# Kernel tuning notes

Measured on AMD Instinct MI355X. Metric: run time of the kernel, lower is better.

Reference implementation:

```python
import jax, jax.numpy as jnp
import numpy as np

B, T, D, V, MEM = 2, 512, 512, 256, 256


def _gru(x, h0, wih, whh, bih, bhh):
    # x: [B,T,D], h0: [B,D]; torch GRU gate order: r, z, n
    def step(h, xt):
        gi = xt @ wih.T + bih            # [B,3D]
        gh = h @ whh.T + bhh             # [B,3D]
        i_r, i_z, i_n = jnp.split(gi, 3, axis=-1)
        h_r, h_z, h_n = jnp.split(gh, 3, axis=-1)
        r = jax.nn.sigmoid(i_r + h_r)
        z = jax.nn.sigmoid(i_z + h_z)
        n = jnp.tanh(i_n + r * h_n)
        h_new = (1.0 - z) * n + z * h
        return h_new, h_new
    hT, ys = jax.lax.scan(step, h0, jnp.swapaxes(x, 0, 1))
    return jnp.swapaxes(ys, 0, 1), hT


def _layernorm(x, g, b, eps=1e-5):
    m = jnp.mean(x, axis=-1, keepdims=True)
    v = jnp.mean((x - m) ** 2, axis=-1, keepdims=True)
    return (x - m) / jnp.sqrt(v + eps) * g + b


def setup_inputs() -> dict:
    key = jax.random.key(0)
    ks = jax.random.split(key, 24)
    s = 1.0 / np.sqrt(D)
    inp = {
        'x': jax.random.randint(ks[0], (B, T), 0, V, dtype=jnp.int32),
        'h_f': jnp.zeros((1, B, D), jnp.float32),
        'h_s': jnp.zeros((1, B, D), jnp.float32),
        'soma_w': jax.random.normal(ks[1], (V, D), jnp.float32),
        'fast_wih': jax.random.normal(ks[2], (3 * D, D)) * s,
        'fast_whh': jax.random.normal(ks[3], (3 * D, D)) * s,
        'fast_bih': jax.random.normal(ks[4], (3 * D,)) * s,
        'fast_bhh': jax.random.normal(ks[5], (3 * D,)) * s,
        'slow_wih': jax.random.normal(ks[6], (3 * D, D)) * s,
        'slow_whh': jax.random.normal(ks[7], (3 * D, D)) * s,
        'slow_bih': jax.random.normal(ks[8], (3 * D,)) * s,
        'slow_bhh': jax.random.normal(ks[9], (3 * D,)) * s,
        'qkv_w': jax.random.normal(ks[10], (3 * D, D)) * s,
        'qkv_b': jax.random.normal(ks[11], (3 * D,)) * s,
        'gate_w': jax.random.normal(ks[12], (D, D)) * s,
        'gate_b': jax.random.normal(ks[13], (D,)) * s,
        'gate_g': jnp.ones((D,), jnp.float32),
        'gate_bb': jnp.zeros((D,), jnp.float32),
        'mem_bank': jax.random.normal(ks[14], (MEM, D)) * 0.1,
        'hip_qw': jax.random.normal(ks[15], (D, D)) * s,
        'hip_qb': jax.random.normal(ks[16], (D,)) * s,
        'axon_w': jax.random.normal(ks[17], (D, 4 * D)) * (0.5 * s),
        'axon_b': jax.random.normal(ks[18], (D,)) * s,
        'norm_g': jnp.ones((D,), jnp.float32),
        'norm_b': jnp.zeros((D,), jnp.float32),
    }
    return inp


def reference(x, h_f, h_s, soma_w, fast_wih, fast_whh, fast_bih, fast_bhh,
              slow_wih, slow_whh, slow_bih, slow_bhh, qkv_w, qkv_b,
              gate_w, gate_b, gate_g, gate_bb, mem_bank, hip_qw, hip_qb,
              axon_w, axon_b, norm_g, norm_b):
    d = soma_w.shape[1]
    s_in = soma_w[x]  # mod[0] == 1.0
    p_f, hf1 = _gru(s_in, h_f[0], fast_wih, fast_whh, fast_bih, fast_bhh)
    p_s, hs1 = _gru(p_f, h_s[0], slow_wih, slow_whh, slow_bih, slow_bhh)
    # LinearIntentMemory: naive cumulative outer-product linear attention
    qkv = p_s @ qkv_w.T + qkv_b
    q, k, v = jnp.split(qkv, 3, axis=-1)
    q = jax.nn.elu(q) + 1.0
    k = jax.nn.elu(k) + 1.0
    kv_cum = jnp.cumsum(jnp.einsum('bti,btj->btij', k, v), axis=1)  # [B,T,D,D]
    num = jnp.einsum('bti,btij->btj', q, kv_cum)
    den = jnp.einsum('bti,bti->bt', q, jnp.cumsum(k, axis=1))[..., None] + 1e-6
    l_mem = num / den
    # intent gate: Linear -> LayerNorm -> Tanh
    intent = jnp.tanh(_layernorm(p_s @ gate_w.T + gate_b, gate_g, gate_bb))
    # hippocampus: softmax attention over memory bank
    qh = p_s @ hip_qw.T + hip_qb
    attn = qh @ mem_bank.T / jnp.sqrt(jnp.float32(d))
    episodes = jax.nn.softmax(attn, axis=-1) @ mem_bank
    combined = jnp.concatenate([p_f, intent, l_mem, episodes], axis=-1)
    thought = _layernorm(jnp.tanh(combined @ axon_w.T + axon_b), norm_g, norm_b)
    sw = soma_w / jnp.maximum(jnp.linalg.norm(soma_w, axis=-1, keepdims=True), 1e-12)
    logits = (thought @ sw.T) * 16.0
    return (logits, thought, hf1[None], hs1[None])
```

## Files before the change

kernel.cpp:

```cpp
#include <hip/hip_runtime.h>
#include <cstddef>

#define F_ELUQK 1
#define F_CAUSAL 2
#define F_DIV 4
#define F_NN 8
#define F_SCALE 16
#define F_ROWSUM 32
#define FLAG_STRIDE 32
#define L_WGS 64
#define UNITS 8

enum : int {
  OFF_QH = 0,
  OFF_COMB = 524288,
  OFF_PS = OFF_COMB + 2097152,
  OFF_QKV = OFF_PS + 524288,
  OFF_SCORES = OFF_QKV + 1572864,
  OFF_DEN = OFF_SCORES + 524288,
  OFF_TMP = OFF_DEN + 1024,
  OFF_ATTN = OFF_TMP + 524288,
  OFF_SWN = OFF_ATTN + 262144,
  OFF_RING = OFF_SWN + 256,
  OFF_HSB = OFF_RING + 4096,
  OFF_FLAGS = OFF_HSB + 2048
};

__global__ __launch_bounds__(256) void gemm(
    const float* __restrict__ A, int lda, const float* __restrict__ B, int ldb,
    float* __restrict__ C, int ldc, int coff, int K,
    const float* __restrict__ bias, const float* __restrict__ den,
    const float* __restrict__ cscale, float* __restrict__ rsum,
    float scale, int flags, int bBatch,
    float* __restrict__ Cz, int kzoff) {
  __shared__ float As[16 * 65];
  __shared__ float Bs[16 * 65];
  int tid = threadIdx.x;
  int n0 = blockIdx.x * 64, m0 = blockIdx.y * 64;
  if (blockIdx.z) { A += kzoff; B += kzoff; C = Cz; bias = nullptr; }
  int rowoff = (m0 >> 9) * bBatch;
  int tx = tid & 15, ty = tid >> 4;

  if ((flags & F_CAUSAL) && n0 > ((m0 & 511) + 63)) {
    #pragma unroll
    for (int i = 0; i < 4; ++i)
      #pragma unroll
      for (int j = 0; j < 4; ++j)
        C[(size_t)(m0 + ty * 4 + i) * ldc + coff + n0 + tx * 4 + j] = 0.f;
    return;
  }

  float acc[4][4] = {};
  for (int k0 = 0; k0 < K; k0 += 16) {
    {
      int rr = tid >> 2, c4 = (tid & 3) << 2;
      const float* ap = A + (size_t)(m0 + rr) * lda + (k0 + c4);
      float4 av = *(const float4*)ap;
      As[(c4 + 0) * 65 + rr] = av.x;
      As[(c4 + 1) * 65 + rr] = av.y;
      As[(c4 + 2) * 65 + rr] = av.z;
      As[(c4 + 3) * 65 + rr] = av.w;
    }
    if (!(flags & F_NN)) {
      int rr = tid >> 2, c4 = (tid & 3) << 2;
      const float* bp = B + (size_t)(n0 + rr + rowoff) * ldb + (k0 + c4);
      float4 bv = *(const float4*)bp;
      Bs[(c4 + 0) * 65 + rr] = bv.x; Bs[(c4 + 1) * 65 + rr] = bv.y;
      Bs[(c4 + 2) * 65 + rr] = bv.z; Bs[(c4 + 3) * 65 + rr] = bv.w;
    } else {
      int kk = tid >> 4, n4 = (tid & 15) << 2;
      const float* bp = B + (size_t)(k0 + kk + rowoff) * ldb + (n0 + n4);
      float4 bv = *(const float4*)bp;
      Bs[kk * 65 + n4 + 0] = bv.x; Bs[kk * 65 + n4 + 1] = bv.y;
      Bs[kk * 65 + n4 + 2] = bv.z; Bs[kk * 65 + n4 + 3] = bv.w;
    }
    __syncthreads();
    #pragma unroll
    for (int k = 0; k < 16; ++k) {
      float av[4], bv[4];
      #pragma unroll
      for (int i = 0; i < 4; ++i) av[i] = As[k * 65 + ty * 4 + i];
      #pragma unroll
      for (int j = 0; j < 4; ++j) bv[j] = Bs[k * 65 + tx * 4 + j];
      #pragma unroll
      for (int i = 0; i < 4; ++i)
        #pragma unroll
        for (int j = 0; j < 4; ++j)
          acc[i][j] = fmaf(av[i], bv[j], acc[i][j]);
    }
    __syncthreads();
  }
  float rs[4] = {0.f, 0.f, 0.f, 0.f};
  #pragma unroll
  for (int i = 0; i < 4; ++i) {
    int m = m0 + ty * 4 + i;
    float dv = (flags & F_DIV) ? (1.0f / (den[m] + 1e-6f)) : 1.0f;
    #pragma unroll
    for (int j = 0; j < 4; ++j) {
      int n = n0 + tx * 4 + j;
      float v = acc[i][j];
      if (bias) v += bias[n];
      if (flags & F_ELUQK) { if (n < 1024) v = (v > 0.f) ? (v + 1.f) : __expf(v); }
      if (flags & F_CAUSAL) { if (n > (m & 511)) v = 0.f; }
      if (flags & F_SCALE) v *= scale;
      if (cscale) v *= cscale[coff + n];
      if (flags & F_DIV) v *= dv;
      C[(size_t)m * ldc + coff + n] = v;
      if (flags & F_ROWSUM) rs[i] += v;
    }
  }
  if (flags & F_ROWSUM) {
    #pragma unroll
    for (int i = 0; i < 4; ++i) {
      float s = rs[i];
      s += __shfl_xor(s, 1); s += __shfl_xor(s, 2);
      s += __shfl_xor(s, 4); s += __shfl_xor(s, 8);
      if (tx == 0) atomicAdd(rsum + (m0 + ty * 4 + i), s);
    }
  }
}

__global__ __launch_bounds__(256) void gemm3(
    const float* __restrict__ A,
    const float* __restrict__ qkvw, const float* __restrict__ qkvb,
    const float* __restrict__ gatew, const float* __restrict__ gateb,
    const float* __restrict__ hipw, const float* __restrict__ hipb,
    float* __restrict__ QKV, float* __restrict__ TMP, float* __restrict__ QH) {
  __shared__ float As[16 * 65];
  __shared__ float Bs[16 * 65];
  int tid = threadIdx.x;
  int n0 = blockIdx.x * 64, m0 = blockIdx.y * 64;
  const float* B; const float* bias; float* C; int ldc, base;
  if (n0 < 1536) { B = qkvw; bias = qkvb; C = QKV; ldc = 1536; base = 0; }
  else if (n0 < 2048) { B = gatew; bias = gateb; C = TMP; ldc = 512; base = 1536; }
  else { B = hipw; bias = hipb; C = QH; ldc = 512; base = 2048; }
  int tx = tid & 15, ty = tid >> 4;
  float acc[4][4] = {};
  for (int k0 = 0; k0 < 512; k0 += 16) {
    {
      int rr = tid >> 2, c4 = (tid & 3) << 2;
      const float* ap = A + (size_t)(m0 + rr) * 512 + (k0 + c4);
      float4 av = *(const float4*)ap;
      As[(c4 + 0) * 65 + rr] = av.x; As[(c4 + 1) * 65 + rr] = av.y;
      As[(c4 + 2) * 65 + rr] = av.z; As[(c4 + 3) * 65 + rr] = av.w;
    }
    {
      int rr = tid >> 2, c4 = (tid & 3) << 2;
      const float* bp = B + (size_t)(n0 - base + rr) * 512 + (k0 + c4);
      float4 bv = *(const float4*)bp;
      Bs[(c4 + 0) * 65 + rr] = bv.x; Bs[(c4 + 1) * 65 + rr] = bv.y;
      Bs[(c4 + 2) * 65 + rr] = bv.z; Bs[(c4 + 3) * 65 + rr] = bv.w;
    }
    __syncthreads();
    #pragma unroll
    for (int k = 0; k < 16; ++k) {
      float av[4], bv[4];
      #pragma unroll
      for (int i = 0; i < 4; ++i) av[i] = As[k * 65 + ty * 4 + i];
      #pragma unroll
      for (int j = 0; j < 4; ++j) bv[j] = Bs[k * 65 + tx * 4 + j];
      #pragma unroll
      for (int i = 0; i < 4; ++i)
        #pragma unroll
        for (int j = 0; j < 4; ++j)
          acc[i][j] = fmaf(av[i], bv[j], acc[i][j]);
    }
    __syncthreads();
  }
  #pragma unroll
  for (int i = 0; i < 4; ++i) {
    int m = m0 + ty * 4 + i;
    #pragma unroll
    for (int j = 0; j < 4; ++j) {
      int n = n0 + tx * 4 + j;
      float v = acc[i][j] + bias[n - base];
      if (n < 1024) v = (v > 0.f) ? (v + 1.f) : __expf(v);
      C[(size_t)m * ldc + (n - base)] = v;
    }
  }
}

__device__ __forceinline__ void post_flag(unsigned* flags, int w, unsigned v) {
  __hip_atomic_store(flags + (size_t)w * FLAG_STRIDE, v, __ATOMIC_RELAXED,
                     __HIP_MEMORY_SCOPE_AGENT);
}
__device__ __forceinline__ void poll64(const unsigned* flags, unsigned tgt, int lane) {
  const unsigned* p = flags + (size_t)lane * FLAG_STRIDE;
  while (__hip_atomic_load(p, __ATOMIC_RELAXED, __HIP_MEMORY_SCOPE_AGENT) < tgt)
    __builtin_amdgcn_s_sleep(1);
}

__global__ __launch_bounds__(256, 1) void gru2_kernel(
    const float* __restrict__ soma, const int* __restrict__ x,
    const float* __restrict__ fwih, const float* __restrict__ fbih,
    const float* __restrict__ fwhh, const float* __restrict__ fbhh,
    const float* __restrict__ h0f,
    const float* __restrict__ swih, const float* __restrict__ sbih,
    const float* __restrict__ swhh, const float* __restrict__ sbhh,
    const float* __restrict__ h0s,
    float* __restrict__ pf_out,
    float* __restrict__ ps_out,
    float* __restrict__ hfT, float* __restrict__ hsT,
    float* __restrict__ ring,
    float* __restrict__ hsbuf,
    unsigned* __restrict__ flagsA, unsigned* __restrict__ flagsB) {
  __shared__ __attribute__((aligned(16))) float hl[1024];
  __shared__ __attribute__((aligned(16))) float inb[2048];
  __shared__ float P[48];
  __shared__ float Q[48];
  __shared__ float bl[24];
  __shared__ float bi[24];
  __shared__ int xl[1024];
  int tid = threadIdx.x, wg = blockIdx.x;
  bool L1 = wg < L_WGS;
  int j0 = (wg & (L_WGS - 1)) * UNITS;
  int part = tid & 7, r = tid >> 3;
  int g = r >> 3, u = r & 7;
  int wave = tid >> 6, lane = tid & 63;
  const float* whh = L1 ? fwhh : swhh;
  const float* bhh = L1 ? fbhh : sbhh;
  const float* wih = L1 ? fwih : swih;
  const float* bih = L1 ? fbih : sbih;

  float4 wh[16], wi[16];
  if (r < 24) {
    const float* wp = whh + (size_t)(g * 512 + j0 + u) * 512 + part * 4;
    #pragma unroll
    for (int i = 0; i < 16; ++i) wh[i] = *(const float4*)(wp + i * 32);
    const float* wp2 = wih + (size_t)(g * 512 + j0 + u) * 512 + part * 4;
    #pragma unroll
    for (int i = 0; i < 16; ++i) wi[i] = *(const float4*)(wp2 + i * 32);
  }
  if (tid < 24) {
    bl[tid] = bhh[(tid >> 3) * 512 + j0 + (tid & 7)];
    bi[tid] = bih[(tid >> 3) * 512 + j0 + (tid & 7)];
  }
  if (L1) {
    for (int q = tid; q < 1024; q += 256) xl[q] = x[q];
  }
  __syncthreads();

  unsigned long long* hlq = (unsigned long long*)hl;
  unsigned long long* inq = (unsigned long long*)inb;
  const float4* h4 = (const float4*)hl;

  if (L1) {
    for (int t = 0; t < 512; ++t) {
      if (wave == 0) {
        if (t > 0) poll64(flagsA, (unsigned)t, lane);
        unsigned long long v[8];
        if (t == 0) {
          const unsigned long long* s8 = (const unsigned long long*)h0f;
          #pragma unroll
          for (int k = 0; k < 8; ++k) v[k] = s8[k * 64 + lane];
        } else {
          const unsigned long long* s8 =
              (const unsigned long long*)(ring + ((t - 1) & 3) * 1024);
          #pragma unroll
          for (int k = 0; k < 8; ++k)
            v[k] = __hip_atomic_load(s8 + k * 64 + lane, __ATOMIC_RELAXED,
                                     __HIP_MEMORY_SCOPE_AGENT);
        }
        #pragma unroll
        for (int k = 0; k < 8; ++k) hlq[k * 64 + lane] = v[k];
      } else if (wave == 1) {
        if (t >= 4) poll64(flagsB, (unsigned)(t - 3), lane);
      } else {
        int b = wave - 2;
        if (t == 0) {
          int row0 = xl[b * 512];
          const float4* sp = (const float4*)(soma + (size_t)row0 * 512);
          float4* dst = (float4*)(inb + b * 512);
          dst[lane * 2] = sp[lane * 2]; dst[lane * 2 + 1] = sp[lane * 2 + 1];
        }
        if (t + 1 < 512) {
          int row = xl[b * 512 + t + 1];
          const float4* sp = (const float4*)(soma + (size_t)row * 512);
          float4* dst = (float4*)(inb + ((t + 1) & 1) * 1024 + b * 512);
          dst[lane * 2] = sp[lane * 2]; dst[lane * 2 + 1] = sp[lane * 2 + 1];
        }
      }
      __syncthreads();
      if (r < 24) {
        const float4* f4v = (const float4*)(inb + (t & 1) * 1024);
        float a0 = 0.f, a1 = 0.f, c0 = 0.f, c1 = 0.f;
        #pragma unroll
        for (int i = 0; i < 16; ++i) {
          float4 w = wh[i];
          float4 x0 = h4[i * 8 + part];
          float4 x1 = h4[128 + i * 8 + part];
          a0 += w.x * x0.x + w.y * x0.y + w.z * x0.z + w.w * x0.w;
          a1 += w.x * x1.x + w.y * x1.y + w.z * x1.z + w.w * x1.w;
          float4 v = wi[i];
          float4 y0 = f4v[i * 8 + part];
          float4 y1 = f4v[128 + i * 8 + part];
          c0 += v.x * y0.x + v.y * y0.y + v.z * y0.z + v.w * y0.w;
          c1 += v.x * y1.x + v.y * y1.y + v.z * y1.z + v.w * y1.w;
        }
        a0 += __shfl_xor(a0, 1); a0 += __shfl_xor(a0, 2); a0 += __shfl_xor(a0, 4);
        a1 += __shfl_xor(a1, 1); a1 += __shfl_xor(a1, 2); a1 += __shfl_xor(a1, 4);
        c0 += __shfl_xor(c0, 1); c0 += __shfl_xor(c0, 2); c0 += __shfl_xor(c0, 4);
        c1 += __shfl_xor(c1, 1); c1 += __shfl_xor(c1, 2); c1 += __shfl_xor(c1, 4);
        if (part == 0) { P[r] = a0; P[24 + r] = a1; Q[r] = c0; Q[24 + r] = c1; }
      }
      __syncthreads();
      if (tid < 16) {
        int b = tid >> 3, u2 = tid & 7, j = j0 + u2;
        float i_r = Q[b * 24 + u2] + bi[u2];
        float i_z = Q[b * 24 + 8 + u2] + bi[8 + u2];
        float i_n = Q[b * 24 + 16 + u2] + bi[16 + u2];
        float gh_r = P[b * 24 + u2] + bl[u2];
        float gh_z = P[b * 24 + 8 + u2] + bl[8 + u2];
        float gh_n = P[b * 24 + 16 + u2] + bl[16 + u2];
        float hold = hl[b * 512 + j];
        float rg = 1.0f / (1.0f + __expf(-(i_r + gh_r)));
        float zg = 1.0f / (1.0f + __expf(-(i_z + gh_z)));
        float ng = tanhf(i_n + rg * gh_n);
        float hnew = (1.0f - zg) * ng + zg * hold;
        __hip_atomic_store(ring + (size_t)(t & 3) * 1024 + b * 512 + j, hnew,
                           __ATOMIC_RELAXED, __HIP_MEMORY_SCOPE_AGENT);
        pf_out[(size_t)(b * 512 + t) * 2048 + j] = hnew;
        if (t == 511) hfT[b * 512 + j] = hnew;
      }
      __syncthreads();
      if (tid == 0) post_flag(flagsA, wg, (unsigned)(t + 1));
    }
  } else {
    for (int t2 = 0; t2 < 512; ++t2) {
      if (wave == 0) {
        poll64(flagsA, (unsigned)(t2 + 1), lane);
        const unsigned long long* f8 =
            (const unsigned long long*)(ring + (t2 & 3) * 1024);
        unsigned long long v[8];
        #pragma unroll
        for (int k = 0; k < 8; ++k)
          v[k] = __hip_atomic_load(f8 + k * 64 + lane, __ATOMIC_RELAXED,
                                   __HIP_MEMORY_SCOPE_AGENT);
        #pragma unroll
        for (int k = 0; k < 8; ++k) inq[(t2 & 1) * 512 + k * 64 + lane] = v[k];
      } else if (wave == 1) {
        unsigned long long v[8];
        if (t2 == 0) {
          const unsigned long long* s8 = (const unsigned long long*)h0s;
          #pragma unroll
          for (int k = 0; k < 8; ++k) v[k] = s8[k * 64 + lane];
        } else {
          poll64(flagsB, (unsigned)t2, lane);
          const unsigned long long* s8 =
              (const unsigned long long*)(hsbuf + ((t2 - 1) & 1) * 1024);
          #pragma unroll
          for (int k = 0; k < 8; ++k)
            v[k] = __hip_atomic_load(s8 + k * 64 + lane, __ATOMIC_RELAXED,
                                     __HIP_MEMORY_SCOPE_AGENT);
        }
        #pragma unroll
        for (int k = 0; k < 8; ++k) hlq[k * 64 + lane] = v[k];
      }
      __syncthreads();
      if (r < 24) {
        const float4* f4v = (const float4*)(inb + (t2 & 1) * 1024);
        float a0 = 0.f, a1 = 0.f, c0 = 0.f, c1 = 0.f;
        #pragma unroll
        for (int i = 0; i < 16; ++i) {
          float4 w = wh[i];
          float4 x0 = h4[i * 8 + part];
          float4 x1 = h4[128 + i * 8 + part];
          a0 += w.x * x0.x + w.y * x0.y + w.z * x0.z + w.w * x0.w;
          a1 += w.x * x1.x + w.y * x1.y + w.z * x1.z + w.w * x1.w;
          float4 v = wi[i];
          float4 y0 = f4v[i * 8 + part];
          float4 y1 = f4v[128 + i * 8 + part];
          c0 += v.x * y0.x + v.y * y0.y + v.z * y0.z + v.w * y0.w;
          c1 += v.x * y1.x + v.y * y1.y + v.z * y1.z + v.w * y1.w;
        }
        a0 += __shfl_xor(a0, 1); a0 += __shfl_xor(a0, 2); a0 += __shfl_xor(a0, 4);
        a1 += __shfl_xor(a1, 1); a1 += __shfl_xor(a1, 2); a1 += __shfl_xor(a1, 4);
        c0 += __shfl_xor(c0, 1); c0 += __shfl_xor(c0, 2); c0 += __shfl_xor(c0, 4);
        c1 += __shfl_xor(c1, 1); c1 += __shfl_xor(c1, 2); c1 += __shfl_xor(c1, 4);
        if (part == 0) { P[r] = a0; P[24 + r] = a1; Q[r] = c0; Q[24 + r] = c1; }
      }
      __syncthreads();
      if (tid < 16) {
        int b = tid >> 3, u2 = tid & 7, j = j0 + u2;
        float i_r = Q[b * 24 + u2] + bi[u2];
        float i_z = Q[b * 24 + 8 + u2] + bi[8 + u2];
        float i_n = Q[b * 24 + 16 + u2] + bi[16 + u2];
        float gh_r = P[b * 24 + u2] + bl[u2];
        float gh_z = P[b * 24 + 8 + u2] + bl[8 + u2];
        float gh_n = P[b * 24 + 16 + u2] + bl[16 + u2];
        float hold = hl[b * 512 + j];
        float rg = 1.0f / (1.0f + __expf(-(i_r + gh_r)));
        float zg = 1.0f / (1.0f + __expf(-(i_z + gh_z)));
        float ng = tanhf(i_n + rg * gh_n);
        float hnew = (1.0f - zg) * ng + zg * hold;
        __hip_atomic_store(hsbuf + (size_t)(t2 & 1) * 1024 + b * 512 + j, hnew,
                           __ATOMIC_RELAXED, __HIP_MEMORY_SCOPE_AGENT);
        ps_out[(size_t)(b * 512 + t2) * 512 + j] = hnew;
        if (t2 == 511) hsT[b * 512 + j] = hnew;
      }
      __syncthreads();
      if (tid == 0) post_flag(flagsB, wg - L_WGS, (unsigned)(t2 + 1));
    }
  }
}

__global__ __launch_bounds__(256) void softmax_kernel(float* __restrict__ a) {
  int m = blockIdx.x, tid = threadIdx.x;
  float v = a[(size_t)m * 256 + tid];
  float mx = v;
  #pragma unroll
  for (int off = 32; off > 0; off >>= 1) mx = fmaxf(mx, __shfl_down(mx, off));
  __shared__ float r4[4];
  __shared__ float s4[4];
  if ((tid & 63) == 0) r4[tid >> 6] = mx;
  __syncthreads();
  mx = fmaxf(fmaxf(r4[0], r4[1]), fmaxf(r4[2], r4[3]));
  float e = __expf(v - mx);
  float s = e;
  #pragma unroll
  for (int off = 32; off > 0; off >>= 1) s += __shfl_down(s, off);
  if ((tid & 63) == 0) s4[tid >> 6] = s;
  __syncthreads();
  s = s4[0] + s4[1] + s4[2] + s4[3];
  a[(size_t)m * 256 + tid] = e / s;
}

__global__ __launch_bounds__(256) void ln_kernel(
    const float* __restrict__ src, const float* __restrict__ src2,
    float* __restrict__ dst, int ldd, int dcoff,
    const float* __restrict__ gv, const float* __restrict__ bv, int tanhFirst) {
  int m = blockIdx.x, tid = threadIdx.x;
  float x0 = src[(size_t)m * 512 + tid];
  float x1 = src[(size_t)m * 512 + 256 + tid];
  if (src2) { x0 += src2[(size_t)m * 512 + tid]; x1 += src2[(size_t)m * 512 + 256 + tid]; }
  if (tanhFirst) { x0 = tanhf(x0); x1 = tanhf(x1); }
  float s = x0 + x1, ss = x0 * x0 + x1 * x1;
  #pragma unroll
  for (int off = 32; off > 0; off >>= 1) { s += __shfl_down(s, off); ss += __shfl_down(ss, off); }
  __shared__ float rs[4], rss[4];
  if ((tid & 63) == 0) { rs[tid >> 6] = s; rss[tid >> 6] = ss; }
  __syncthreads();
  float st = rs[0] + rs[1] + rs[2] + rs[3];
  float sst = rss[0] + rss[1] + rss[2] + rss[3];
  float mean = st * (1.0f / 512.0f);
  float var = sst * (1.0f / 512.0f) - mean * mean;
  float inv = rsqrtf(var + 1e-5f);
  float y0 = (x0 - mean) * inv * gv[tid] + bv[tid];
  float y1 = (x1 - mean) * inv * gv[256 + tid] + bv[256 + tid];
  if (!tanhFirst) { y0 = tanhf(y0); y1 = tanhf(y1); }
  dst[(size_t)m * ldd + dcoff + tid] = y0;
  dst[(size_t)m * ldd + dcoff + 256 + tid] = y1;
}

__global__ __launch_bounds__(256) void swinv_kernel(const float* __restrict__ soma,
                                                    float* __restrict__ swn) {
  int r = blockIdx.x, tid = threadIdx.x;
  float x0 = soma[(size_t)r * 512 + tid];
  float x1 = soma[(size_t)r * 512 + 256 + tid];
  float ss = x0 * x0 + x1 * x1;
  #pragma unroll
  for (int off = 32; off > 0; off >>= 1) ss += __shfl_down(ss, off);
  __shared__ float r4[4];
  if ((tid & 63) == 0) r4[tid >> 6] = ss;
  __syncthreads();
  if (tid == 0) {
    float norm = fmaxf(sqrtf(r4[0] + r4[1] + r4[2] + r4[3]), 1e-12f);
    swn[r] = 16.0f / norm;
  }
}

extern "C" void kernel_launch(void* const* d_in, const int* in_sizes, int n_in,
                              void* d_out, int out_size, void* d_ws, size_t ws_size,
                              hipStream_t stream) {
  (void)in_sizes; (void)n_in; (void)out_size; (void)ws_size;
  float* W = (float*)d_ws;
  float* outf = (float*)d_out;
  const int* x = (const int*)d_in[0];
  const float* soma = (const float*)d_in[3];

  hipMemsetAsync((char*)d_ws + (size_t)OFF_FLAGS * 4, 0, 16384, stream);
  hipMemsetAsync((char*)d_ws + (size_t)OFF_DEN * 4, 0, 4096, stream);

  gru2_kernel<<<2 * L_WGS, 256, 0, stream>>>(soma, x,
      (const float*)d_in[4], (const float*)d_in[6],
      (const float*)d_in[5], (const float*)d_in[7], (const float*)d_in[1],
      (const float*)d_in[8], (const float*)d_in[10],
      (const float*)d_in[9], (const float*)d_in[11], (const float*)d_in[2],
      W + OFF_COMB, W + OFF_PS, outf + 786432, outf + 787456,
      W + OFF_RING, W + OFF_HSB,
      (unsigned*)(W + OFF_FLAGS), (unsigned*)(W + OFF_FLAGS) + L_WGS * FLAG_STRIDE);

  gemm3<<<dim3(40, 16), 256, 0, stream>>>(W + OFF_PS,
      (const float*)d_in[12], (const float*)d_in[13],
      (const float*)d_in[14], (const float*)d_in[15],
      (const float*)d_in[19], (const float*)d_in[20],
      W + OFF_QKV, W + OFF_TMP, W + OFF_QH);

  gemm<<<dim3(8, 16), 256, 0, stream>>>(W + OFF_QKV, 1536, W + OFF_QKV + 512, 1536,
      W + OFF_SCORES, 512, 0, 512, nullptr, nullptr, nullptr, W + OFF_DEN,
      1.f, F_CAUSAL | F_ROWSUM, 512, nullptr, 0);

  gemm<<<dim3(8, 16), 256, 0, stream>>>(W + OFF_SCORES, 512, W + OFF_QKV + 1024, 1536,
      W + OFF_COMB, 2048, 1024, 512, nullptr, W + OFF_DEN, nullptr, nullptr,
      1.f, F_NN | F_DIV, 512, nullptr, 0);

  ln_kernel<<<1024, 256, 0, stream>>>(W + OFF_TMP, nullptr, W + OFF_COMB, 2048, 512,
      (const float*)d_in[16], (const float*)d_in[17], 0);

  gemm<<<dim3(4, 16), 256, 0, stream>>>(W + OFF_QH, 512, (const float*)d_in[18], 512,
      W + OFF_ATTN, 256, 0, 512, nullptr, nullptr, nullptr, nullptr,
      0.04419417382415922f, F_SCALE, 0, nullptr, 0);
  softmax_kernel<<<1024, 256, 0, stream>>>(W + OFF_ATTN);
  gemm<<<dim3(8, 16), 256, 0, stream>>>(W + OFF_ATTN, 256, (const float*)d_in[18], 512,
      W + OFF_COMB, 2048, 1536, 256, nullptr, nullptr, nullptr, nullptr,
      1.f, F_NN, 0, nullptr, 0);

  gemm<<<dim3(8, 16, 2), 256, 0, stream>>>(W + OFF_COMB, 2048, (const float*)d_in[21], 2048,
      W + OFF_TMP, 512, 0, 1024, (const float*)d_in[22], nullptr, nullptr, nullptr,
      1.f, 0, 0, W + OFF_QH, 1024);

  ln_kernel<<<1024, 256, 0, stream>>>(W + OFF_TMP, W + OFF_QH, outf + 262144, 512, 0,
      (const float*)d_in[23], (const float*)d_in[24], 1);

  swinv_kernel<<<256, 256, 0, stream>>>(soma, W + OFF_SWN);
  gemm<<<dim3(4, 16), 256, 0, stream>>>(outf + 262144, 512, soma, 512,
      outf, 256, 0, 512, nullptr, nullptr, W + OFF_SWN, nullptr,
      1.f, 0, 0, nullptr, 0);
}
```

Baseline: 2.025 ms.

## Replace flag-based step handoff with step-tagged hidden-state words in GRU ring

Each hidden-state value is now stored as a 64-bit word that packs the float with its step number. Consumers poll the data words directly until every tag matches the step they expect. This removes the separate release-flag round trip and one __syncthreads per step in the persistent cross-workgroup GRU recurrence. In exchange the ring and buffer traffic doubles in size, and polling now re-reads 16 words per lane instead of one flag. The slow layer now posts its consumption flag as soon as it has read the fast ring, rather than at the end of the step.

```diff
diff --git a/kernel.cpp b/kernel.cpp
--- a/kernel.cpp
+++ b/kernel.cpp
@@ -22,8 +22,8 @@
   OFF_ATTN = OFF_TMP + 524288,
   OFF_SWN = OFF_ATTN + 262144,
   OFF_RING = OFF_SWN + 256,
-  OFF_HSB = OFF_RING + 4096,
-  OFF_FLAGS = OFF_HSB + 2048
+  OFF_HSB = OFF_RING + 8192,
+  OFF_FLAGS = OFF_HSB + 4096
 };
 
 __global__ __launch_bounds__(256) void gemm(
@@ -201,9 +201,9 @@
     float* __restrict__ pf_out,
     float* __restrict__ ps_out,
     float* __restrict__ hfT, float* __restrict__ hsT,
-    float* __restrict__ ring,
-    float* __restrict__ hsbuf,
-    unsigned* __restrict__ flagsA, unsigned* __restrict__ flagsB) {
+    unsigned long long* __restrict__ ringq,
+    unsigned long long* __restrict__ hsq,
+    unsigned* __restrict__ flagsB) {
   __shared__ __attribute__((aligned(16))) float hl[1024];
   __shared__ __attribute__((aligned(16))) float inb[2048];
   __shared__ float P[48];
@@ -240,29 +240,33 @@
   }
   __syncthreads();
 
-  unsigned long long* hlq = (unsigned long long*)hl;
-  unsigned long long* inq = (unsigned long long*)inb;
   const float4* h4 = (const float4*)hl;
 
   if (L1) {
     for (int t = 0; t < 512; ++t) {
       if (wave == 0) {
-        if (t > 0) poll64(flagsA, (unsigned)t, lane);
-        unsigned long long v[8];
         if (t == 0) {
-          const unsigned long long* s8 = (const unsigned long long*)h0f;
           #pragma unroll
-          for (int k = 0; k < 8; ++k) v[k] = s8[k * 64 + lane];
+          for (int k = 0; k < 16; ++k) hl[k * 64 + lane] = h0f[k * 64 + lane];
         } else {
-          const unsigned long long* s8 =
-              (const unsigned long long*)(ring + ((t - 1) & 3) * 1024);
+          const unsigned long long* s8 = ringq + (size_t)((t - 1) & 3) * 1024;
+          unsigned expect = (unsigned)t;
+          unsigned long long v[16];
+          for (;;) {
+            #pragma unroll
+            for (int k = 0; k < 16; ++k)
+              v[k] = __hip_atomic_load(s8 + k * 64 + lane, __ATOMIC_RELAXED,
+                                       __HIP_MEMORY_SCOPE_AGENT);
+            unsigned bad = 0;
+            #pragma unroll
+            for (int k = 0; k < 16; ++k) bad |= ((unsigned)(v[k] >> 32)) ^ expect;
+            if (__all(bad == 0)) break;
+            __builtin_amdgcn_s_sleep(1);
+          }
           #pragma unroll
-          for (int k = 0; k < 8; ++k)
-            v[k] = __hip_atomic_load(s8 + k * 64 + lane, __ATOMIC_RELAXED,
-                                     __HIP_MEMORY_SCOPE_AGENT);
-        }
-        #pragma unroll
-        for (int k = 0; k < 8; ++k) hlq[k * 64 + lane] = v[k];
+          for (int k = 0; k < 16; ++k)
+            hl[k * 64 + lane] = __uint_as_float((unsigned)v[k]);
+        }
       } else if (wave == 1) {
         if (t >= 4) poll64(flagsB, (unsigned)(t - 3), lane);
       } else {
@@ -317,44 +321,60 @@
         float zg = 1.0f / (1.0f + __expf(-(i_z + gh_z)));
         float ng = tanhf(i_n + rg * gh_n);
         float hnew = (1.0f - zg) * ng + zg * hold;
-        __hip_atomic_store(ring + (size_t)(t & 3) * 1024 + b * 512 + j, hnew,
+        unsigned long long pv =
+            ((unsigned long long)(unsigned)(t + 1) << 32) |
+            (unsigned long long)__float_as_uint(hnew);
+        __hip_atomic_store(ringq + (size_t)(t & 3) * 1024 + b * 512 + j, pv,
                            __ATOMIC_RELAXED, __HIP_MEMORY_SCOPE_AGENT);
         pf_out[(size_t)(b * 512 + t) * 2048 + j] = hnew;
         if (t == 511) hfT[b * 512 + j] = hnew;
       }
-      __syncthreads();
-      if (tid == 0) post_flag(flagsA, wg, (unsigned)(t + 1));
+      __asm__ __volatile__("s_barrier" ::: "memory");
     }
   } else {
     for (int t2 = 0; t2 < 512; ++t2) {
       if (wave == 0) {
-        poll64(flagsA, (unsigned)(t2 + 1), lane);
-        const unsigned long long* f8 =
-            (const unsigned long long*)(ring + (t2 & 3) * 1024);
-        unsigned long long v[8];
+        const unsigned long long* f8 = ringq + (size_t)(t2 & 3) * 1024;
+        unsigned expect = (unsigned)(t2 + 1);
+        unsigned long long v[16];
+        for (;;) {
+          #pragma unroll
+          for (int k = 0; k < 16; ++k)
+            v[k] = __hip_atomic_load(f8 + k * 64 + lane, __ATOMIC_RELAXED,
+                                     __HIP_MEMORY_SCOPE_AGENT);
+          unsigned bad = 0;
+          #pragma unroll
+          for (int k = 0; k < 16; ++k) bad |= ((unsigned)(v[k] >> 32)) ^ expect;
+          if (__all(bad == 0)) break;
+          __builtin_amdgcn_s_sleep(1);
+        }
         #pragma unroll
-        for (int k = 0; k < 8; ++k)
-          v[k] = __hip_atomic_load(f8 + k * 64 + lane, __ATOMIC_RELAXED,
-                                   __HIP_MEMORY_SCOPE_AGENT);
-        #pragma unroll
-        for (int k = 0; k < 8; ++k) inq[(t2 & 1) * 512 + k * 64 + lane] = v[k];
+        for (int k = 0; k < 16; ++k)
+          inb[(t2 & 1) * 1024 + k * 64 + lane] = __uint_as_float((unsigned)v[k]);
+        if (lane == 0) post_flag(flagsB, wg - L_WGS, (unsigned)(t2 + 1));
       } else if (wave == 1) {
-        unsigned long long v[8];
         if (t2 == 0) {
-          const unsigned long long* s8 = (const unsigned long long*)h0s;
           #pragma unroll
-          for (int k = 0; k < 8; ++k) v[k] = s8[k * 64 + lane];
+          for (int k = 0; k < 16; ++k) hl[k * 64 + lane] = h0s[k * 64 + lane];
         } else {
-          poll64(flagsB, (unsigned)t2, lane);
-          const unsigned long long* s8 =
-              (const unsigned long long*)(hsbuf + ((t2 - 1) & 1) * 1024);
+          const unsigned long long* s8 = hsq + (size_t)((t2 - 1) & 1) * 1024;
+          unsigned expect = (unsigned)t2;
+          unsigned long long v[16];
+          for (;;) {
+            #pragma unroll
+            for (int k = 0; k < 16; ++k)
+              v[k] = __hip_atomic_load(s8 + k * 64 + lane, __ATOMIC_RELAXED,
+                                       __HIP_MEMORY_SCOPE_AGENT);
+            unsigned bad = 0;
+            #pragma unroll
+            for (int k = 0; k < 16; ++k) bad |= ((unsigned)(v[k] >> 32)) ^ expect;
+            if (__all(bad == 0)) break;
+            __builtin_amdgcn_s_sleep(1);
+          }
           #pragma unroll
-          for (int k = 0; k < 8; ++k)
-            v[k] = __hip_atomic_load(s8 + k * 64 + lane, __ATOMIC_RELAXED,
-                                     __HIP_MEMORY_SCOPE_AGENT);
-        }
-        #pragma unroll
-        for (int k = 0; k < 8; ++k) hlq[k * 64 + lane] = v[k];
+          for (int k = 0; k < 16; ++k)
+            hl[k * 64 + lane] = __uint_as_float((unsigned)v[k]);
+        }
       }
       __syncthreads();
       if (r < 24) {
@@ -393,13 +413,15 @@
         float zg = 1.0f / (1.0f + __expf(-(i_z + gh_z)));
         float ng = tanhf(i_n + rg * gh_n);
         float hnew = (1.0f - zg) * ng + zg * hold;
-        __hip_atomic_store(hsbuf + (size_t)(t2 & 1) * 1024 + b * 512 + j, hnew,
+        unsigned long long pv =
+            ((unsigned long long)(unsigned)(t2 + 1) << 32) |
+            (unsigned long long)__float_as_uint(hnew);
+        __hip_atomic_store(hsq + (size_t)(t2 & 1) * 1024 + b * 512 + j, pv,
                            __ATOMIC_RELAXED, __HIP_MEMORY_SCOPE_AGENT);
         ps_out[(size_t)(b * 512 + t2) * 512 + j] = hnew;
         if (t2 == 511) hsT[b * 512 + j] = hnew;
       }
-      __syncthreads();
-      if (tid == 0) post_flag(flagsB, wg - L_WGS, (unsigned)(t2 + 1));
+      __asm__ __volatile__("s_barrier" ::: "memory");
     }
   }
 }
@@ -478,7 +500,7 @@
   const int* x = (const int*)d_in[0];
   const float* soma = (const float*)d_in[3];
 
-  hipMemsetAsync((char*)d_ws + (size_t)OFF_FLAGS * 4, 0, 16384, stream);
+  hipMemsetAsync((char*)d_ws + (size_t)OFF_RING * 4, 0, 57344, stream);
   hipMemsetAsync((char*)d_ws + (size_t)OFF_DEN * 4, 0, 4096, stream);
 
   gru2_kernel<<<2 * L_WGS, 256, 0, stream>>>(soma, x,
@@ -487,8 +509,8 @@
       (const float*)d_in[8], (const float*)d_in[10],
       (const float*)d_in[9], (const float*)d_in[11], (const float*)d_in[2],
       W + OFF_COMB, W + OFF_PS, outf + 786432, outf + 787456,
-      W + OFF_RING, W + OFF_HSB,
-      (unsigned*)(W + OFF_FLAGS), (unsigned*)(W + OFF_FLAGS) + L_WGS * FLAG_STRIDE);
+      (unsigned long long*)(W + OFF_RING), (unsigned long long*)(W + OFF_HSB),
+      (unsigned*)(W + OFF_FLAGS));
 
   gemm3<<<dim3(40, 16), 256, 0, stream>>>(W + OFF_PS,
       (const float*)d_in[12], (const float*)d_in[13],
```

Result: slower. 2.104 ms (+3.9%).
